# Performance work log

Hardware: AMD Instinct MI355X
Metric: run time of the kernel (lower is better)

## Reference

```python
import jax, jax.numpy as jnp
import numpy as np

HIDDEN = 1024
NUM_HEAD = 16
HEAD_DIM = HIDDEN // NUM_HEAD


def setup_inputs() -> dict:
    key = jax.random.key(0)
    ks = jax.random.split(key, 9)
    B, S = 1, 4096
    scale = 1.0 / np.sqrt(HIDDEN)
    inp = {
        "x": jax.random.normal(ks[0], (B, S, HIDDEN), dtype=jnp.float32),
        "wq": jax.random.normal(ks[1], (HIDDEN, HIDDEN), dtype=jnp.float32) * scale,
        "bq": jnp.zeros((HIDDEN,), dtype=jnp.float32),
        "wk": jax.random.normal(ks[2], (HIDDEN, HIDDEN), dtype=jnp.float32) * scale,
        "bk": jnp.zeros((HIDDEN,), dtype=jnp.float32),
        "wv": jax.random.normal(ks[3], (HIDDEN, HIDDEN), dtype=jnp.float32) * scale,
        "bv": jnp.zeros((HIDDEN,), dtype=jnp.float32),
        "wo": jax.random.normal(ks[4], (HIDDEN, HIDDEN), dtype=jnp.float32) * scale,
        "bo": jnp.zeros((HIDDEN,), dtype=jnp.float32),
    }
    return inp


def reference(x, wq, bq, wk, bk, wv, bv, wo, bo):
    B, S, _ = x.shape
    # QKV projections (torch Linear: x @ W.T + b)
    def split_heads(t):
        return t.reshape(B, S, NUM_HEAD, HEAD_DIM).transpose(0, 2, 1, 3)  # [B,H,S,D]
    q = split_heads(x @ wq.T + bq)
    k = split_heads(x @ wk.T + bk)
    v = split_heads(x @ wv.T + bv)
    # scaled dot-product scores: [B,H,S,S]
    scores = jnp.einsum('bhsd,bhtd->bhst', q, k) / jnp.sqrt(jnp.float32(HEAD_DIM))
    # faithful double softmax over the key axis (no mask; dropout = eval identity)
    attn = jax.nn.softmax(scores, axis=-1)
    attn = jax.nn.softmax(attn, axis=-1)
    out = jnp.einsum('bhst,bhtd->bhsd', attn, v)  # [B,H,S,D]
    out = out.transpose(0, 2, 1, 3).reshape(B, S, HIDDEN)
    return out @ wo.T + bo
```

## Files before the change

### kernel.cpp

```cpp
#include <hip/hip_runtime.h>
#include <hip/hip_bf16.h>
#include <stdint.h>

#define S 4096
#define HID 1024
#define NH 16
#define DH 64

typedef __attribute__((ext_vector_type(4))) short s16x4;
typedef __attribute__((ext_vector_type(8))) short short8;
typedef __attribute__((ext_vector_type(4))) float f32x4;
typedef __attribute__((ext_vector_type(16))) float f32x16;

__device__ __forceinline__ unsigned short f2bf(float f) {
  unsigned int u = __builtin_bit_cast(unsigned int, f);
  u += 0x7FFF + ((u >> 16) & 1);
  return (unsigned short)(u >> 16);
}
__device__ __forceinline__ unsigned int pktrunc(float lo, float hi) {
  return __builtin_amdgcn_perm(__builtin_bit_cast(unsigned int, hi),
                               __builtin_bit_cast(unsigned int, lo), 0x07060302u);
}
__device__ __forceinline__ void gload16(const unsigned short* g, unsigned short* l) {
  __builtin_amdgcn_global_load_lds((const __attribute__((address_space(1))) unsigned int*)g,
                                   (__attribute__((address_space(3))) unsigned int*)l, 16, 0, 0);
}

__global__ __launch_bounds__(256) void cast_kernel(
    const float* __restrict__ x,  const float* __restrict__ wq,
    const float* __restrict__ wk, const float* __restrict__ wv,
    const float* __restrict__ wo,
    unsigned short* __restrict__ xb,  unsigned short* __restrict__ wqb,
    unsigned short* __restrict__ wkb, unsigned short* __restrict__ wvb,
    unsigned short* __restrict__ wob)
{
  int y = blockIdx.y;
  const float* src; unsigned short* dst; int n;
  if      (y == 0) { src = x;  dst = xb;  n = S * HID; }
  else if (y == 1) { src = wq; dst = wqb; n = HID * HID; }
  else if (y == 2) { src = wk; dst = wkb; n = HID * HID; }
  else if (y == 3) { src = wv; dst = wvb; n = HID * HID; }
  else             { src = wo; dst = wob; n = HID * HID; }
  int i = (blockIdx.x * 256 + threadIdx.x) * 4;
  if (i < n) {
    float4 v = *reinterpret_cast<const float4*>(src + i);
    ushort4 o;
    o.x = f2bf(v.x); o.y = f2bf(v.y); o.z = f2bf(v.z); o.w = f2bf(v.w);
    *reinterpret_cast<ushort4*>(dst + i) = o;
  }
}

__device__ __forceinline__ void gemm128(
    const unsigned short* __restrict__ A, const unsigned short* __restrict__ W,
    unsigned short* As, unsigned short* Bs, f32x4 acc[4][4], int row0, int col0)
{
  const int tid = threadIdx.x;
  const int wave = tid >> 6, lane = tid & 63, quad = lane >> 4, l16 = lane & 15;
  const int wr = (wave >> 1) * 64, wc = (wave & 1) * 64;
  const int srow = lane >> 2, sseg = lane & 3;
  const f32x4 z = {0.f, 0.f, 0.f, 0.f};
  #pragma unroll
  for (int i = 0; i < 4; i++)
    #pragma unroll
    for (int j = 0; j < 4; j++) acc[i][j] = z;

  for (int k0 = 0; k0 < HID; k0 += 32) {
    __syncthreads();
    #pragma unroll
    for (int c = 0; c < 2; c++) {
      const int rbase = c * 64 + wave * 16;
      gload16(A + (size_t)(row0 + rbase + srow) * HID + k0 + sseg * 8, As + rbase * 32);
      gload16(W + (size_t)(col0 + rbase + srow) * HID + k0 + sseg * 8, Bs + rbase * 32);
    }
    __syncthreads();

    short8 af[4], bfr[4];
    #pragma unroll
    for (int i = 0; i < 4; i++)
      af[i] = *reinterpret_cast<const short8*>(As + (wr + i * 16 + l16) * 32 + quad * 8);
    #pragma unroll
    for (int j = 0; j < 4; j++)
      bfr[j] = *reinterpret_cast<const short8*>(Bs + (wc + j * 16 + l16) * 32 + quad * 8);
    #pragma unroll
    for (int i = 0; i < 4; i++)
      #pragma unroll
      for (int j = 0; j < 4; j++)
        acc[i][j] = __builtin_amdgcn_mfma_f32_16x16x32_bf16(af[i], bfr[j], acc[i][j], 0, 0, 0);
  }
}

__global__ __launch_bounds__(256) void qkv_gemm_kernel(
    const unsigned short* __restrict__ X,
    const unsigned short* __restrict__ Wq, const unsigned short* __restrict__ Wk,
    const unsigned short* __restrict__ Wv,
    const float* __restrict__ bq, const float* __restrict__ bk, const float* __restrict__ bv,
    unsigned short* __restrict__ Qo, unsigned short* __restrict__ K2o, unsigned short* __restrict__ Vbo)
{
  __shared__ unsigned short As[128 * 32];
  __shared__ unsigned short Bs[128 * 32];
  const int zsel = blockIdx.z;
  const unsigned short* W = (zsel == 0) ? Wq : (zsel == 1) ? Wk : Wv;
  const float* bias        = (zsel == 0) ? bq : (zsel == 1) ? bk : bv;
  const int row0 = blockIdx.x * 128, col0 = blockIdx.y * 128;
  f32x4 acc[4][4];
  gemm128(X, W, As, Bs, acc, row0, col0);

  const int tid = threadIdx.x;
  const int wave = tid >> 6, lane = tid & 63, quad = lane >> 4, l16 = lane & 15;
  const int wr = (wave >> 1) * 64, wc = (wave & 1) * 64;

  if (zsel == 0) {
    const float osc = 0.18033688011112042f;
    #pragma unroll
    for (int j = 0; j < 4; j++) {
      int n = col0 + wc + j * 16 + l16;
      float bb = bias[n];
      int h = n >> 6, d = n & 63;
      #pragma unroll
      for (int i = 0; i < 4; i++)
        #pragma unroll
        for (int rr = 0; rr < 4; rr++) {
          int s = row0 + wr + i * 16 + quad * 4 + rr;
          Qo[(size_t)(h * S + s) * DH + d] = f2bf((acc[i][j][rr] + bb) * osc);
        }
    }
  } else if (zsel == 1) {
    #pragma unroll
    for (int j = 0; j < 4; j++) {
      int n = col0 + wc + j * 16 + l16;
      float bb = bias[n];
      int h = n >> 6, dh = n & 63;
      int c = dh >> 4, hfk = (dh >> 3) & 1, j8 = dh & 7;
      #pragma unroll
      for (int i = 0; i < 4; i++)
        #pragma unroll
        for (int rr = 0; rr < 4; rr++) {
          int s = row0 + wr + i * 16 + quad * 4 + rr;
          int g = s >> 5, l32k = s & 31;
          K2o[((size_t)((h * 128 + g) * 4 + c) * 64 + hfk * 32 + l32k) * 8 + j8] =
              f2bf(acc[i][j][rr] + bb);
        }
    }
  } else {
    #pragma unroll
    for (int j = 0; j < 4; j++) {
      int n = col0 + wc + j * 16 + l16;
      float bb = bias[n];
      int h = n >> 6, dh = n & 63;
      int ng = dh >> 5, l32v = dh & 31;
      #pragma unroll
      for (int i = 0; i < 4; i++) {
        int sb = row0 + wr + i * 16 + quad * 4;
        int kw = sb >> 3, hfb = (sb >> 2) & 1;
        ushort4 pv;
        pv.x = f2bf(acc[i][j][0] + bb); pv.y = f2bf(acc[i][j][1] + bb);
        pv.z = f2bf(acc[i][j][2] + bb); pv.w = f2bf(acc[i][j][3] + bb);
        *reinterpret_cast<ushort4*>(
            Vbo + ((size_t)(((h * 512 + kw) * 2 + ng) * 2 + hfb) * 32 + l32v) * 4) = pv;
      }
    }
  }
}

__global__ __launch_bounds__(256) void out_gemm_kernel(
    const unsigned short* __restrict__ A, const unsigned short* __restrict__ W,
    const float* __restrict__ be, float* __restrict__ dst)
{
  __shared__ unsigned short As[128 * 32];
  __shared__ unsigned short Bs[128 * 32];
  const int row0 = blockIdx.x * 128, col0 = blockIdx.y * 128;
  f32x4 acc[4][4];
  gemm128(A, W, As, Bs, acc, row0, col0);

  const int tid = threadIdx.x;
  const int wave = tid >> 6, lane = tid & 63, quad = lane >> 4, l16 = lane & 15;
  const int wr = (wave >> 1) * 64, wc = (wave & 1) * 64;
  #pragma unroll
  for (int j = 0; j < 4; j++) {
    int n = col0 + wc + j * 16 + l16;
    float bb = be[n];
    #pragma unroll
    for (int i = 0; i < 4; i++)
      #pragma unroll
      for (int rr = 0; rr < 4; rr++) {
        int s = row0 + wr + i * 16 + quad * 4 + rr;
        dst[(size_t)s * HID + n] = acc[i][j][rr] + bb;
      }
  }
}

__global__ __launch_bounds__(256) void vsum_kernel(
    const unsigned short* __restrict__ Vb, float* __restrict__ VsumP)
{
  __shared__ float red[256];
  const int p = blockIdx.x, h = blockIdx.y, tid = threadIdx.x;
  const int d = tid & 63, chunk = tid >> 6;
  const int ng = d >> 5, l32 = d & 31;
  float s = 0.f;
  for (int m = 0; m < 16; m++) {
    int kw = p * 64 + chunk * 16 + m;
    #pragma unroll
    for (int hfb = 0; hfb < 2; hfb++) {
      uint2 u = *reinterpret_cast<const uint2*>(
          Vb + ((size_t)(((h * 512 + kw) * 2 + ng) * 2 + hfb) * 32 + l32) * 4);
      s += __builtin_bit_cast(float, u.x << 16);
      s += __builtin_bit_cast(float, u.x & 0xFFFF0000u);
      s += __builtin_bit_cast(float, u.y << 16);
      s += __builtin_bit_cast(float, u.y & 0xFFFF0000u);
    }
  }
  red[tid] = s;
  __syncthreads();
  if (tid < 64)
    VsumP[p * 1024 + h * 64 + tid] = red[tid] + red[64 + tid] + red[128 + tid] + red[192 + tid];
}

__global__ __launch_bounds__(256) void biasfold_kernel(
    const float* __restrict__ VsumP, const float* __restrict__ wo,
    const float* __restrict__ bo, float* __restrict__ be)
{
  const int n = blockIdx.x * 4 + (threadIdx.x >> 6);
  const int l = threadIdx.x & 63;
  float acc = 0.f;
  #pragma unroll
  for (int i = 0; i < 16; i++) {
    float vs = 0.f;
    #pragma unroll
    for (int p = 0; p < 8; p++) vs += VsumP[p * 1024 + l + 64 * i];
    acc += vs * wo[(size_t)n * HID + l + 64 * i];
  }
  #pragma unroll
  for (int off = 32; off >= 1; off >>= 1) acc += __shfl_xor(acc, off);
  if (l == 0) be[n] = bo[n] + acc * (1.f / 4097.f);
}

__global__ __launch_bounds__(256, 4) void attn_kernel(
    const unsigned short* __restrict__ Q, const unsigned short* __restrict__ K2,
    const unsigned short* __restrict__ Vb, unsigned short* __restrict__ OUT)
{
  __shared__ float Ol[2][32][64];
  __shared__ float Z1l[128];

  const int h = blockIdx.y, q0 = blockIdx.x * 64;
  const int tid = threadIdx.x;
  const int wave = tid >> 6, lane = tid & 63, hf = lane >> 5, l32 = lane & 31;
  const int qc = wave & 1, ks = wave >> 1;

  short8 qf[4];
  {
    const unsigned short* qrow = Q + (size_t)(h * S + q0 + qc * 32 + l32) * DH;
    #pragma unroll
    for (int c = 0; c < 4; c++)
      qf[c] = *reinterpret_cast<const short8*>(qrow + c * 16 + hf * 8);
  }

  float z1p = 0.f;
  f32x16 Oa[2];
  #pragma unroll
  for (int ng = 0; ng < 2; ng++)
    #pragma unroll
    for (int r = 0; r < 16; r++) Oa[ng][r] = 0.f;

  const int g0 = ks * 64, g1 = g0 + 64;
  for (int g = g0; g < g1; g++) {
    short8 kf[4];
    #pragma unroll
    for (int c = 0; c < 4; c++)
      kf[c] = *reinterpret_cast<const short8*>(
          K2 + ((size_t)((h * 128 + g) * 4 + c) * 64 + lane) * 8);
    s16x4 vf[4][2];
    #pragma unroll
    for (int w2 = 0; w2 < 4; w2++)
      #pragma unroll
      for (int ng = 0; ng < 2; ng++)
        vf[w2][ng] = *reinterpret_cast<const s16x4*>(
            Vb + ((size_t)(((h * 512 + g * 4 + w2) * 2 + ng) * 2 + hf) * 32 + l32) * 4);

    f32x16 acc;
    #pragma unroll
    for (int r = 0; r < 16; r++) acc[r] = 0.f;
    #pragma unroll
    for (int c = 0; c < 4; c++)
      acc = __builtin_amdgcn_mfma_f32_32x32x16_bf16(kf[c], qf[c], acc, 0, 0, 0);

    #pragma unroll
    for (int w2 = 0; w2 < 4; w2++) {
      float t0 = __builtin_amdgcn_exp2f(acc[4 * w2 + 0]);
      float t1 = __builtin_amdgcn_exp2f(acc[4 * w2 + 1]);
      float t2 = __builtin_amdgcn_exp2f(acc[4 * w2 + 2]);
      float t3 = __builtin_amdgcn_exp2f(acc[4 * w2 + 3]);
      z1p += (t0 + t1) + (t2 + t3);
      uint2 pa; pa.x = pktrunc(t0, t1); pa.y = pktrunc(t2, t3);
      s16x4 A8 = __builtin_bit_cast(s16x4, pa);
      Oa[0] = __builtin_amdgcn_mfma_f32_32x32x8bf16_1k(A8, vf[w2][0], Oa[0], 0, 0, 0);
      Oa[1] = __builtin_amdgcn_mfma_f32_32x32x8bf16_1k(A8, vf[w2][1], Oa[1], 0, 0, 0);
    }
  }

  {
    float z1 = z1p + __shfl_xor(z1p, 32);
    if (hf == 0) Z1l[ks * 64 + qc * 32 + l32] = z1;
  }
  if (ks == 0) {
    #pragma unroll
    for (int reg = 0; reg < 16; reg++) {
      const int row = (reg & 3) + 8 * (reg >> 2) + 4 * hf;
      #pragma unroll
      for (int ng = 0; ng < 2; ng++)
        Ol[qc][row][ng * 32 + l32] = Oa[ng][reg];
    }
  }
  __syncthreads();
  if (ks == 1) {
    #pragma unroll
    for (int reg = 0; reg < 16; reg++) {
      const int row = (reg & 3) + 8 * (reg >> 2) + 4 * hf;
      const int ql = qc * 32 + row;
      const float rz = 1.f / ((Z1l[ql] + Z1l[64 + ql]) * 4097.f);
      const int s = q0 + ql;
      #pragma unroll
      for (int ng = 0; ng < 2; ng++) {
        const float o = Ol[qc][row][ng * 32 + l32] + Oa[ng][reg];
        OUT[(size_t)s * HID + h * DH + ng * 32 + l32] = f2bf(o * rz);
      }
    }
  }
}

extern "C" void kernel_launch(void* const* d_in, const int* in_sizes, int n_in,
                              void* d_out, int out_size, void* d_ws, size_t ws_size,
                              hipStream_t stream) {
  const float* x  = (const float*)d_in[0];
  const float* wq = (const float*)d_in[1];
  const float* bq = (const float*)d_in[2];
  const float* wk = (const float*)d_in[3];
  const float* bk = (const float*)d_in[4];
  const float* wv = (const float*)d_in[5];
  const float* bv = (const float*)d_in[6];
  const float* wo = (const float*)d_in[7];
  const float* bo = (const float*)d_in[8];
  float* out = (float*)d_out;

  char* ws = (char*)d_ws;
  unsigned short* xb  = (unsigned short*)(ws);
  unsigned short* wqb = (unsigned short*)(ws + (8u  << 20));
  unsigned short* wkb = (unsigned short*)(ws + (10u << 20));
  unsigned short* wvb = (unsigned short*)(ws + (12u << 20));
  unsigned short* wob = (unsigned short*)(ws + (14u << 20));
  unsigned short* qw  = (unsigned short*)(ws + (16u << 20));
  unsigned short* k2  = (unsigned short*)(ws + (24u << 20));
  unsigned short* vb  = (unsigned short*)(ws + (32u << 20));
  float* vsump        = (float*)(ws + (40u << 20));
  float* be           = (float*)(ws + (40u << 20) + 65536);
  unsigned short* aw  = xb;

  cast_kernel<<<dim3(4096, 5), 256, 0, stream>>>(x, wq, wk, wv, wo, xb, wqb, wkb, wvb, wob);
  qkv_gemm_kernel<<<dim3(32, 8, 3), 256, 0, stream>>>(xb, wqb, wkb, wvb, bq, bk, bv, qw, k2, vb);
  vsum_kernel<<<dim3(8, 16), 256, 0, stream>>>(vb, vsump);
  biasfold_kernel<<<dim3(256), 256, 0, stream>>>(vsump, wo, bo, be);
  attn_kernel<<<dim3(64, 16), 256, 0, stream>>>(qw, k2, vb, aw);
  out_gemm_kernel<<<dim3(32, 8, 1), 256, 0, stream>>>(aw, wob, be, out);
}
```

Baseline: 266.7 us.

## Use 32x32x16 bf16 MFMA for PV with repacked V layout

Repacks the V projection output into a layout grouped by 16 keys so that each lane loads 8 bf16 values per fragment. The attention loop then feeds the exponentiated scores straight into four 32x32x16 MFMAs instead of eight 32x32x8 MFMAs, and does half as many V loads at twice the width. The vsum kernel is updated to read the new layout with 16-byte loads. The intent is fewer MFMA issues and fewer, wider memory loads in the hot loop. It depends on the score accumulator register order matching the new V row grouping.

Result: faster. 253.4 us (-5.0%).

```diff
diff --git a/kernel.cpp b/kernel.cpp
--- a/kernel.cpp
+++ b/kernel.cpp
@@ -7,10 +7,10 @@
 #define NH 16
 #define DH 64
 
-typedef __attribute__((ext_vector_type(4))) short s16x4;
 typedef __attribute__((ext_vector_type(8))) short short8;
 typedef __attribute__((ext_vector_type(4))) float f32x4;
 typedef __attribute__((ext_vector_type(16))) float f32x16;
+typedef __attribute__((ext_vector_type(4))) unsigned int u32x4;
 
 __device__ __forceinline__ unsigned short f2bf(float f) {
   unsigned int u = __builtin_bit_cast(unsigned int, f);
@@ -148,15 +148,16 @@
       float bb = bias[n];
       int h = n >> 6, dh = n & 63;
       int ng = dh >> 5, l32v = dh & 31;
+      int hf_v = quad & 1, jj0 = (quad >> 1) * 4;
       #pragma unroll
       for (int i = 0; i < 4; i++) {
-        int sb = row0 + wr + i * 16 + quad * 4;
-        int kw = sb >> 3, hfb = (sb >> 2) & 1;
+        int gt = (row0 + wr + i * 16) >> 5;
+        int grp = i & 1;
         ushort4 pv;
         pv.x = f2bf(acc[i][j][0] + bb); pv.y = f2bf(acc[i][j][1] + bb);
         pv.z = f2bf(acc[i][j][2] + bb); pv.w = f2bf(acc[i][j][3] + bb);
         *reinterpret_cast<ushort4*>(
-            Vbo + ((size_t)(((h * 512 + kw) * 2 + ng) * 2 + hfb) * 32 + l32v) * 4) = pv;
+            Vbo + ((size_t)(((h * 128 + gt) * 2 + grp) * 2 + ng) * 64 + hf_v * 32 + l32v) * 8 + jj0) = pv;
       }
     }
   }
@@ -197,17 +198,21 @@
   const int d = tid & 63, chunk = tid >> 6;
   const int ng = d >> 5, l32 = d & 31;
   float s = 0.f;
-  for (int m = 0; m < 16; m++) {
-    int kw = p * 64 + chunk * 16 + m;
-    #pragma unroll
-    for (int hfb = 0; hfb < 2; hfb++) {
-      uint2 u = *reinterpret_cast<const uint2*>(
-          Vb + ((size_t)(((h * 512 + kw) * 2 + ng) * 2 + hfb) * 32 + l32) * 4);
-      s += __builtin_bit_cast(float, u.x << 16);
-      s += __builtin_bit_cast(float, u.x & 0xFFFF0000u);
-      s += __builtin_bit_cast(float, u.y << 16);
-      s += __builtin_bit_cast(float, u.y & 0xFFFF0000u);
-    }
+  for (int m = 0; m < 4; m++) {
+    int gt = p * 16 + chunk * 4 + m;
+    #pragma unroll
+    for (int grp = 0; grp < 2; grp++)
+      #pragma unroll
+      for (int hf = 0; hf < 2; hf++) {
+        uint4 u = *reinterpret_cast<const uint4*>(
+            Vb + ((size_t)(((h * 128 + gt) * 2 + grp) * 2 + ng) * 64 + hf * 32 + l32) * 8);
+        const unsigned int w[4] = {u.x, u.y, u.z, u.w};
+        #pragma unroll
+        for (int q = 0; q < 4; q++) {
+          s += __builtin_bit_cast(float, w[q] << 16);
+          s += __builtin_bit_cast(float, w[q] & 0xFFFF0000u);
+        }
+      }
   }
   red[tid] = s;
   __syncthreads();
@@ -261,20 +266,22 @@
     #pragma unroll
     for (int r = 0; r < 16; r++) Oa[ng][r] = 0.f;
 
+  const unsigned short* Kb = K2 + (size_t)h * 128 * 4 * 64 * 8;
+  const unsigned short* Vbb = Vb + (size_t)h * 128 * 4 * 64 * 8;
+
   const int g0 = ks * 64, g1 = g0 + 64;
   for (int g = g0; g < g1; g++) {
     short8 kf[4];
     #pragma unroll
     for (int c = 0; c < 4; c++)
-      kf[c] = *reinterpret_cast<const short8*>(
-          K2 + ((size_t)((h * 128 + g) * 4 + c) * 64 + lane) * 8);
-    s16x4 vf[4][2];
-    #pragma unroll
-    for (int w2 = 0; w2 < 4; w2++)
+      kf[c] = *reinterpret_cast<const short8*>(Kb + ((size_t)(g * 4 + c) * 64 + lane) * 8);
+    short8 vfr[2][2];
+    #pragma unroll
+    for (int grp = 0; grp < 2; grp++)
       #pragma unroll
       for (int ng = 0; ng < 2; ng++)
-        vf[w2][ng] = *reinterpret_cast<const s16x4*>(
-            Vb + ((size_t)(((h * 512 + g * 4 + w2) * 2 + ng) * 2 + hf) * 32 + l32) * 4);
+        vfr[grp][ng] = *reinterpret_cast<const short8*>(
+            Vbb + ((size_t)((g * 2 + grp) * 2 + ng) * 64 + lane) * 8);
 
     f32x16 acc;
     #pragma unroll
@@ -283,18 +290,23 @@
     for (int c = 0; c < 4; c++)
       acc = __builtin_amdgcn_mfma_f32_32x32x16_bf16(kf[c], qf[c], acc, 0, 0, 0);
 
-    #pragma unroll
-    for (int w2 = 0; w2 < 4; w2++) {
-      float t0 = __builtin_amdgcn_exp2f(acc[4 * w2 + 0]);
-      float t1 = __builtin_amdgcn_exp2f(acc[4 * w2 + 1]);
-      float t2 = __builtin_amdgcn_exp2f(acc[4 * w2 + 2]);
-      float t3 = __builtin_amdgcn_exp2f(acc[4 * w2 + 3]);
-      z1p += (t0 + t1) + (t2 + t3);
-      uint2 pa; pa.x = pktrunc(t0, t1); pa.y = pktrunc(t2, t3);
-      s16x4 A8 = __builtin_bit_cast(s16x4, pa);
-      Oa[0] = __builtin_amdgcn_mfma_f32_32x32x8bf16_1k(A8, vf[w2][0], Oa[0], 0, 0, 0);
-      Oa[1] = __builtin_amdgcn_mfma_f32_32x32x8bf16_1k(A8, vf[w2][1], Oa[1], 0, 0, 0);
-    }
+    unsigned int D[8];
+    #pragma unroll
+    for (int m = 0; m < 8; m++) {
+      float t0 = __builtin_amdgcn_exp2f(acc[2 * m]);
+      float t1 = __builtin_amdgcn_exp2f(acc[2 * m + 1]);
+      z1p += t0 + t1;
+      D[m] = pktrunc(t0, t1);
+    }
+    u32x4 d0 = {D[0], D[1], D[2], D[3]};
+    u32x4 d1 = {D[4], D[5], D[6], D[7]};
+    short8 A0 = __builtin_bit_cast(short8, d0);
+    short8 A1 = __builtin_bit_cast(short8, d1);
+
+    Oa[0] = __builtin_amdgcn_mfma_f32_32x32x16_bf16(A0, vfr[0][0], Oa[0], 0, 0, 0);
+    Oa[1] = __builtin_amdgcn_mfma_f32_32x32x16_bf16(A0, vfr[0][1], Oa[1], 0, 0, 0);
+    Oa[0] = __builtin_amdgcn_mfma_f32_32x32x16_bf16(A1, vfr[1][0], Oa[0], 0, 0, 0);
+    Oa[1] = __builtin_amdgcn_mfma_f32_32x32x16_bf16(A1, vfr[1][1], Oa[1], 0, 0, 0);
   }
 
   {
```
